# Optimization experiments

Hardware: AMD Instinct MI355X
Metric: run time of the kernel (lower is better)

The kernel has to match this reference:

```python
import jax, jax.numpy as jnp
import numpy as np

HEAD, DIM, R = 8, 256, 3
RA = (2 * R + 1) ** 2  # 49


def conv2d(x, w, b=None, pad=0, groups=1):
    y = jax.lax.conv_general_dilated(x, w, (1, 1), [(pad, pad), (pad, pad)],
                                     dimension_numbers=('NCHW', 'OIHW', 'NCHW'),
                                     feature_group_count=groups)
    return y if b is None else y + b[None, :, None, None]


def grid_sample(img, grid, mode, padding='zeros'):
    # img [B,C,H,W]; grid [B,Hg,Wg,2] with (x,y) in [-1,1]; align_corners=False.
    B, C, H, W = img.shape
    Hg, Wg = grid.shape[1], grid.shape[2]
    gx = ((grid[..., 0] + 1.0) * W - 1.0) / 2.0
    gy = ((grid[..., 1] + 1.0) * H - 1.0) / 2.0
    if padding == 'border':
        gx = jnp.clip(gx, 0.0, W - 1.0)
        gy = jnp.clip(gy, 0.0, H - 1.0)
    gx = gx.reshape(B, -1)
    gy = gy.reshape(B, -1)

    def gather(iy, ix):
        iyc = jnp.clip(iy, 0, H - 1)
        ixc = jnp.clip(ix, 0, W - 1)
        return jax.vmap(lambda im, a, b: im[:, a, b])(img, iyc, ixc)  # [B,C,N]

    def mask(iy, ix):
        if padding == 'border':
            return jnp.ones(iy.shape, img.dtype)
        return ((ix >= 0) & (ix < W) & (iy >= 0) & (iy < H)).astype(img.dtype)

    if mode == 'nearest':
        ix = jnp.round(gx).astype(jnp.int32)
        iy = jnp.round(gy).astype(jnp.int32)
        out = gather(iy, ix) * mask(iy, ix)[:, None, :]
    else:  # bilinear
        x0f = jnp.floor(gx); y0f = jnp.floor(gy)
        wx = gx - x0f; wy = gy - y0f
        x0 = x0f.astype(jnp.int32); y0 = y0f.astype(jnp.int32)
        out = jnp.zeros((B, C, gx.shape[1]), img.dtype)
        for dx, dy, w in ((0, 0, (1 - wx) * (1 - wy)), (1, 0, wx * (1 - wy)),
                          (0, 1, (1 - wx) * wy), (1, 1, wx * wy)):
            ix = x0 + dx; iy = y0 + dy
            out = out + gather(iy, ix) * (w * mask(iy, ix))[:, None, :]
    return out.reshape(B, C, Hg, Wg)


def mlp2(x, W1, b1, W2, b2):
    return jax.nn.relu(x @ W1.T + b1) @ W2.T + b2


def setup_inputs() -> dict:
    key = jax.random.key(0)
    ks = jax.random.split(key, 32)
    B, H, W, Q = 1, 64, 64, 4096
    f32 = jnp.float32
    rn = lambda k, shp, s=0.02: jax.random.normal(k, shp, f32) * s
    return {
        'inp': jax.random.normal(ks[0], (B, 3, H, W), f32),
        'coord': jax.random.uniform(ks[1], (B, Q, 2), f32, -1.0, 1.0),
        'cell': jnp.full((B, Q, 2), 2.0 / (2 * H), f32),
        'W_enc': rn(ks[2], (64, 3, 3, 3)), 'b_enc': jnp.zeros((64,), f32),
        'W_ch': rn(ks[3], (256, 64, 3, 3)), 'b_ch': jnp.zeros((256,), f32),
        'W_q': rn(ks[4], (256, 256, 3, 3)), 'b_q': jnp.zeros((256,), f32),
        'W_k': rn(ks[5], (256, 256, 3, 3)), 'b_k': jnp.zeros((256,), f32),
        'W_v': rn(ks[6], (256, 256, 3, 3)), 'b_v': jnp.zeros((256,), f32),
        'W_off1': rn(ks[7], (256, 32, 5, 5)), 'b_off1': jnp.zeros((256,), f32),
        'ln_g': jnp.ones((256,), f32), 'ln_b': jnp.zeros((256,), f32),
        'W_off2': rn(ks[8], (98, 256, 1, 1)),
        'Wc1': rn(ks[9], (256, 98)), 'bc1': jnp.zeros((256,), f32),
        'Wc2': rn(ks[10], (49, 256)), 'bc2': jnp.zeros((49,), f32),
        'Wi1': rn(ks[11], (256, 12546)), 'bi1': jnp.zeros((256,), f32),
        'Wi2': rn(ks[12], (3, 256)), 'bi2': jnp.zeros((3,), f32),
        'scale': 2,
    }


def reference(inp, coord, cell, W_enc, b_enc, W_ch, b_ch, W_q, b_q, W_k, b_k,
              W_v, b_v, W_off1, b_off1, ln_g, ln_b, W_off2, Wc1, bc1, Wc2, bc2,
              Wi1, bi1, Wi2, bi2, scale):
    B, _, H, W = inp.shape
    Q = coord.shape[1]
    # gen_feat: encoder stub (conv+relu) -> conv_ch -> q/k/v convs
    feat = conv2d(jax.nn.relu(conv2d(inp, W_enc, b_enc, pad=1)), W_ch, b_ch, pad=1)
    fq = conv2d(feat, W_q, b_q, pad=1)
    fk = conv2d(feat, W_k, b_k, pad=1)
    fv = conv2d(feat, W_v, b_v, pad=1)
    # offset branch: grouped 5x5 conv -> channelwise LN -> GELU -> 1x1 conv (no bias)
    o = conv2d(feat, W_off1, b_off1, pad=2, groups=8)
    oc = o.transpose(0, 2, 3, 1)
    mu = oc.mean(-1, keepdims=True)
    var = ((oc - mu) ** 2).mean(-1, keepdims=True)
    oc = (oc - mu) / jnp.sqrt(var + 1e-5) * ln_g + ln_b
    offsets = conv2d(jax.nn.gelu(oc.transpose(0, 3, 1, 2), approximate=False), W_off2, None, pad=0)  # [B,98,H,W]
    # LR coordinate grid (y,x) at pixel centers in [-1,1]
    ys = -1.0 + 1.0 / H + (2.0 / H) * jnp.arange(H, dtype=inp.dtype)
    xs = -1.0 + 1.0 / W + (2.0 / W) * jnp.arange(W, dtype=inp.dtype)
    coord_lr = jnp.broadcast_to(jnp.stack(jnp.meshgrid(ys, xs, indexing='ij'), 0)[None], (B, 2, H, W))
    sc = coord[:, :, None, :]          # [B,Q,1,2] (y,x)
    g = sc[..., ::-1]                  # (x,y) for grid_sample
    sck = grid_sample(coord_lr, g, 'nearest').transpose(0, 2, 3, 1)  # [B,Q,1,2]
    off = grid_sample(offsets, g, 'nearest').transpose(0, 2, 3, 1).reshape(B, Q, RA, 2)
    off = jnp.tanh(off) * jnp.array([1.0 / (H - 1.0), 1.0 / (W - 1.0)], inp.dtype) * 2.0
    d = jnp.linspace(-R, R, 2 * R + 1).astype(inp.dtype)
    delta = jnp.stack(jnp.meshgrid(d * (2.0 / H), d * (2.0 / W), indexing='ij'), -1).reshape(1, 1, RA, 2)
    sck = sck + delta + off            # [B,Q,49,2] sampling locs (y,x)
    q = grid_sample(fq, g, 'bilinear').transpose(0, 2, 3, 1).reshape(B, Q, HEAD, DIM // HEAD)
    k = grid_sample(fk, sck[..., ::-1], 'nearest').transpose(0, 2, 3, 1).reshape(B, Q, RA, HEAD, DIM // HEAD)
    v = grid_sample(fv, sck[..., ::-1], 'nearest').transpose(0, 2, 3, 1).reshape(B, Q, RA, HEAD, DIM // HEAD)
    attn_val = jnp.einsum('bqhd,bqkhd->bqkh', q, k) / np.sqrt(DIM // HEAD)  # [B,Q,49,8]
    rel = (sc - sck) * jnp.array([H, W], inp.dtype)  # [B,Q,49,2]
    wcoord = mlp2(rel.reshape(B * Q, RA * 2), Wc1, bc1, Wc2, bc2).reshape(B, Q, RA, 1)
    attn = jax.nn.softmax(wcoord + attn_val, axis=2)  # softmax over 49 samples
    feat_in = (v * attn[..., None]).reshape(B, Q, RA * DIM)
    rel_cell = cell * jnp.array([H, W], inp.dtype)
    feat_in = jnp.concatenate([feat_in, rel_cell], -1)  # [B,Q,12546]
    pred = mlp2(feat_in.reshape(B * Q, -1), Wi1, bi1, Wi2, bi2).reshape(B, Q, 3)
    skip = grid_sample(inp, g, 'bilinear', 'border')[:, :, :, 0].transpose(0, 2, 1)
    return pred + skip
```

## Files before the change

kernel.cpp:

```cpp
#include <hip/hip_runtime.h>
#include <hip/hip_bf16.h>


typedef unsigned short u16;
typedef unsigned int u32;
using frag_ab = __attribute__((ext_vector_type(8))) short;
using frag_cd = __attribute__((ext_vector_type(4))) float;

#define HW 4096
#define NQ 4096
#define KBIG 12576
#define SPLITK 16
#define KCHUNK 800
#define KQ 2304
#define QSPLIT 2
#define QCHUNK 1152

static __device__ __forceinline__ u16 f2b(float f) {
  union { __hip_bfloat16 h; u16 u; } c; c.h = __float2bfloat16(f); return c.u;
}
static __device__ __forceinline__ u32 pk2(float a, float b) {
  union { __hip_bfloat162 h; u32 u; } c;
  c.h = __float22bfloat162_rn(float2{a, b});
  return c.u;
}
static __device__ __forceinline__ void glds16(const u16* g, u16* l) {
  __builtin_amdgcn_global_load_lds(
      (const __attribute__((address_space(1))) u32*)(g),
      (__attribute__((address_space(3))) u32*)(l), 16, 0, 0);
}

#define BM 64
#define BN 64
#define BK 32
#define LDSS 40

__global__ __launch_bounds__(256)
void gemm_bt(const u16* __restrict__ A, const u16* __restrict__ Bt,
             void* __restrict__ Cv, const float* __restrict__ bias,
             int N, int K, int ldc, int flags,
             long sA, long sB, long sC, int sBias)
{
  __shared__ u16 As[BM * LDSS];
  __shared__ u16 Bs[BN * LDSS];
  const int z = blockIdx.z;
  A  += (long)z * sA;
  Bt += (long)z * sB;
  const float* bz = bias ? bias + (long)z * sBias : nullptr;

  const int tid  = threadIdx.x;
  const int m0   = blockIdx.x * BM;
  const int n0   = blockIdx.y * BN;
  const int wave = tid >> 6, lane = tid & 63;
  const int mw = (wave & 1) * 32, nw = (wave >> 1) * 32;
  const int lr = lane & 15, lk = lane >> 4;
  const int srow = tid >> 2, scol = (tid & 3) * 8;

  frag_cd acc[2][2] = {};
  const u16* aptr = A + (size_t)(m0 + srow) * K + scol;
  const bool bok  = (n0 + srow) < N;
  const u16* bptr = Bt + (size_t)(n0 + srow) * K + scol;

  uint4 av = *(const uint4*)(aptr);
  uint4 bv = bok ? *(const uint4*)(bptr) : uint4{0u, 0u, 0u, 0u};

  for (int k0 = 0; k0 < K; k0 += BK) {
    *(uint4*)&As[srow * LDSS + scol] = av;
    *(uint4*)&Bs[srow * LDSS + scol] = bv;
    __syncthreads();
    if (k0 + BK < K) {
      av = *(const uint4*)(aptr + k0 + BK);
      bv = bok ? *(const uint4*)(bptr + k0 + BK) : uint4{0u, 0u, 0u, 0u};
    }
    frag_ab af0 = *(const frag_ab*)&As[(mw      + lr) * LDSS + lk * 8];
    frag_ab af1 = *(const frag_ab*)&As[(mw + 16 + lr) * LDSS + lk * 8];
    frag_ab bf0 = *(const frag_ab*)&Bs[(nw      + lr) * LDSS + lk * 8];
    frag_ab bf1 = *(const frag_ab*)&Bs[(nw + 16 + lr) * LDSS + lk * 8];
    acc[0][0] = __builtin_amdgcn_mfma_f32_16x16x32_bf16(af0, bf0, acc[0][0], 0, 0, 0);
    acc[0][1] = __builtin_amdgcn_mfma_f32_16x16x32_bf16(af0, bf1, acc[0][1], 0, 0, 0);
    acc[1][0] = __builtin_amdgcn_mfma_f32_16x16x32_bf16(af1, bf0, acc[1][0], 0, 0, 0);
    acc[1][1] = __builtin_amdgcn_mfma_f32_16x16x32_bf16(af1, bf1, acc[1][1], 0, 0, 0);
    __syncthreads();
  }

  const bool relu = flags & 1;
  const bool obf  = flags & 2;
  #pragma unroll
  for (int i = 0; i < 2; i++)
    #pragma unroll
    for (int j = 0; j < 2; j++) {
      int col = n0 + nw + j * 16 + lr;
      if (col >= N) continue;
      float badd = bz ? bz[col] : 0.f;
      #pragma unroll
      for (int r = 0; r < 4; r++) {
        int row = m0 + mw + i * 16 + lk * 4 + r;
        float v = acc[i][j][r] + badd;
        if (relu) v = fmaxf(v, 0.f);
        size_t idx = (size_t)z * sC + (size_t)row * ldc + col;
        if (obf) ((u16*)Cv)[idx] = f2b(v);
        else     ((float*)Cv)[idx] = v;
      }
    }
}

template<int W3, int SH, int PAD>
__global__ __launch_bounds__(256)
void gemm_conv(const u16* __restrict__ feat, const u16* __restrict__ Bt,
               void* __restrict__ Cv, const float* __restrict__ bias,
               int N, int K, int ldc, int flags, int FC, int cbStride,
               long sB, long sC, int sBias)
{
  __shared__ u16 As[BM * LDSS];
  __shared__ u16 Bs[BN * LDSS];
  const int z = blockIdx.z;
  Bt += (long)z * sB;
  const float* bz = bias ? bias + (long)z * sBias : nullptr;
  const int cb = z * cbStride;

  const int tid  = threadIdx.x;
  const int m0   = blockIdx.x * BM;
  const int n0   = blockIdx.y * BN;
  const int wave = tid >> 6, lane = tid & 63;
  const int mw = (wave & 1) * 32, nw = (wave >> 1) * 32;
  const int lr = lane & 15, lk = lane >> 4;
  const int srow = tid >> 2, scol = (tid & 3) * 8;
  const int p = m0 + srow, y = p >> 6, x = p & 63;

  frag_cd acc[2][2] = {};
  const bool bok  = (n0 + srow) < N;
  const u16* bptr = Bt + (size_t)(n0 + srow) * K + scol;

  auto stageA = [&](int k0) -> uint4 {
    int k = k0 + scol;
    int s = k >> SH;
    int c = k & ((1 << SH) - 1);
    int dy = s / W3, dx = s - dy * W3;
    int yy = y + dy - PAD, xx = x + dx - PAD;
    if (((unsigned)yy < 64u) && ((unsigned)xx < 64u))
      return *(const uint4*)&feat[(size_t)(yy * 64 + xx) * FC + cb + c];
    return uint4{0u, 0u, 0u, 0u};
  };

  uint4 av = stageA(0);
  uint4 bv = bok ? *(const uint4*)(bptr) : uint4{0u, 0u, 0u, 0u};

  for (int k0 = 0; k0 < K; k0 += BK) {
    *(uint4*)&As[srow * LDSS + scol] = av;
    *(uint4*)&Bs[srow * LDSS + scol] = bv;
    __syncthreads();
    if (k0 + BK < K) {
      av = stageA(k0 + BK);
      bv = bok ? *(const uint4*)(bptr + k0 + BK) : uint4{0u, 0u, 0u, 0u};
    }
    frag_ab af0 = *(const frag_ab*)&As[(mw      + lr) * LDSS + lk * 8];
    frag_ab af1 = *(const frag_ab*)&As[(mw + 16 + lr) * LDSS + lk * 8];
    frag_ab bf0 = *(const frag_ab*)&Bs[(nw      + lr) * LDSS + lk * 8];
    frag_ab bf1 = *(const frag_ab*)&Bs[(nw + 16 + lr) * LDSS + lk * 8];
    acc[0][0] = __builtin_amdgcn_mfma_f32_16x16x32_bf16(af0, bf0, acc[0][0], 0, 0, 0);
    acc[0][1] = __builtin_amdgcn_mfma_f32_16x16x32_bf16(af0, bf1, acc[0][1], 0, 0, 0);
    acc[1][0] = __builtin_amdgcn_mfma_f32_16x16x32_bf16(af1, bf0, acc[1][0], 0, 0, 0);
    acc[1][1] = __builtin_amdgcn_mfma_f32_16x16x32_bf16(af1, bf1, acc[1][1], 0, 0, 0);
    __syncthreads();
  }

  const bool relu = flags & 1;
  const bool obf  = flags & 2;
  #pragma unroll
  for (int i = 0; i < 2; i++)
    #pragma unroll
    for (int j = 0; j < 2; j++) {
      int col = n0 + nw + j * 16 + lr;
      if (col >= N) continue;
      float badd = bz ? bz[col] : 0.f;
      #pragma unroll
      for (int r = 0; r < 4; r++) {
        int row = m0 + mw + i * 16 + lk * 4 + r;
        float v = acc[i][j][r] + badd;
        if (relu) v = fmaxf(v, 0.f);
        size_t idx = (size_t)z * sC + (size_t)row * ldc + col;
        if (obf) ((u16*)Cv)[idx] = f2b(v);
        else     ((float*)Cv)[idx] = v;
      }
    }
}

__global__ __launch_bounds__(256)
void gemm_qkv(const u16* __restrict__ feat, const u16* __restrict__ Bt,
              float* __restrict__ P)
{
  __shared__ u16 As[64 * LDSS];
  __shared__ u16 Bs[128 * 32];
  const int tid  = threadIdx.x;
  const int m0   = blockIdx.x * 64;
  const int n0   = blockIdx.y * 128;
  const int z    = blockIdx.z;
  const int kbeg = z * QCHUNK;
  const int kend = kbeg + QCHUNK;
  const int wave = tid >> 6, lane = tid & 63;
  const int nw = wave * 32;
  const int lr = lane & 15, lk = lane >> 4;
  const int arow = tid >> 2, acol = (tid & 3) * 8;
  const int p = m0 + arow, y = p >> 6, x = p & 63;

  frag_cd acc[4][2] = {};
  const u16* bbase = Bt + (size_t)(n0 + (tid >> 2)) * KQ + (tid & 3) * 8 + kbeg;
  u16* bdst = &Bs[(size_t)tid * 8];

  auto stageA = [&](int k0) -> uint4 {
    int k = k0 + acol;
    int s = k >> 8, c = k & 255;
    int dy = s / 3, dx = s - dy * 3;
    int yy = y + dy - 1, xx = x + dx - 1;
    if (((unsigned)yy < 64u) && ((unsigned)xx < 64u))
      return *(const uint4*)&feat[(size_t)(yy * 64 + xx) * 256 + c];
    return uint4{0u, 0u, 0u, 0u};
  };

  uint4 av = stageA(kbeg);

  for (int k0 = kbeg; k0 < kend; k0 += BK) {
    glds16(bbase + (k0 - kbeg), bdst);
    glds16(bbase + (k0 - kbeg) + (size_t)64 * KQ, bdst + 2048);
    *(uint4*)&As[arow * LDSS + acol] = av;
    __syncthreads();
    if (k0 + BK < kend) av = stageA(k0 + BK);
    frag_ab af[4];
    #pragma unroll
    for (int i = 0; i < 4; i++)
      af[i] = *(const frag_ab*)&As[(i * 16 + lr) * LDSS + lk * 8];
    #pragma unroll
    for (int j = 0; j < 2; j++) {
      frag_ab bf = *(const frag_ab*)&Bs[(nw + j * 16 + lr) * 32 + lk * 8];
      #pragma unroll
      for (int i = 0; i < 4; i++)
        acc[i][j] = __builtin_amdgcn_mfma_f32_16x16x32_bf16(af[i], bf, acc[i][j], 0, 0, 0);
    }
    __syncthreads();
  }

  #pragma unroll
  for (int i = 0; i < 4; i++)
    #pragma unroll
    for (int j = 0; j < 2; j++) {
      int col = n0 + nw + j * 16 + lr;
      #pragma unroll
      for (int r = 0; r < 4; r++) {
        int row = m0 + i * 16 + lk * 4 + r;
        P[(size_t)z * (NQ * 768) + (size_t)row * 768 + col] = acc[i][j][r];
      }
    }
}

__global__ __launch_bounds__(256)
void gemm_big(const u16* __restrict__ Bt, const float* __restrict__ fqkv,
              const float* __restrict__ attnval, const int* __restrict__ vidx,
              const float* __restrict__ cell, float* __restrict__ P)
{
  __shared__ u16 As[64 * LDSS];
  __shared__ u16 Bs[256 * 32];
  __shared__ int   s_vidx[5 * 64];
  __shared__ float s_attn[5 * 64 * 8];
  const int tid  = threadIdx.x;
  const int m0   = blockIdx.x * 64;
  const int z    = blockIdx.y;
  const int kbeg = z * KCHUNK;
  const int kend = min(KBIG, kbeg + KCHUNK);
  const int jbeg = kbeg >> 8;
  const int jcnt = ((kend - 1) >> 8) - jbeg + 1;
  const int wave = tid >> 6, lane = tid & 63;
  const int nw = wave * 64;
  const int lr = lane & 15, lk = lane >> 4;
  const int arow = tid >> 2, acol = (tid & 3) * 8;
  const int q = m0 + arow;

  for (int t = tid; t < 64 * jcnt; t += 256) {
    int r = t & 63, jj = t >> 6;
    int j = jbeg + jj;
    s_vidx[t] = (j < 49) ? vidx[(m0 + r) * 49 + j] : -1;
  }
  for (int t = tid; t < 64 * 8 * jcnt; t += 256) {
    int h = t & 7, rr = (t >> 3) & 63, jj = t >> 9;
    int j = jbeg + jj;
    s_attn[t] = (j < 49) ? attnval[((size_t)((m0 + rr) * 49 + j)) * 8 + h] : 0.f;
  }
  __syncthreads();

  auto stageA = [&](int k0) -> uint4 {
    const int k = k0 + acol;
    const int j = k >> 8, c = k & 255;
    union { u32 w[4]; uint4 v; } r; r.v = uint4{0u, 0u, 0u, 0u};
    if (j < 49) {
      const int jj = j - jbeg;
      int id = s_vidx[jj * 64 + arow];
      if (id >= 0) {
        float w = s_attn[(jj * 64 + arow) * 8 + (c >> 5)];
        const float* src = fqkv + (size_t)id * 768 + 512 + c;
        float4 f0 = *(const float4*)src;
        float4 f1 = *(const float4*)(src + 4);
        r.w[0] = pk2(f0.x * w, f0.y * w);
        r.w[1] = pk2(f0.z * w, f0.w * w);
        r.w[2] = pk2(f1.x * w, f1.y * w);
        r.w[3] = pk2(f1.z * w, f1.w * w);
      }
    } else if (c == 0) {
      r.w[0] = pk2(cell[q * 2] * 64.f, cell[q * 2 + 1] * 64.f);
    }
    return r.v;
  };

  frag_cd acc[4][4] = {};
  uint4 av = stageA(kbeg);
  const u16* bbase = Bt + (size_t)(tid >> 2) * KBIG + (tid & 3) * 8 + kbeg;
  u16* bdst = &Bs[(size_t)tid * 8];

  for (int k0 = kbeg; k0 < kend; k0 += BK) {
    #pragma unroll
    for (int i = 0; i < 4; i++)
      glds16(bbase + (k0 - kbeg) + (size_t)(i * 64) * KBIG, bdst + i * 2048);
    *(uint4*)&As[arow * LDSS + acol] = av;
    __syncthreads();
    if (k0 + BK < kend) av = stageA(k0 + BK);
    frag_ab af[4];
    #pragma unroll
    for (int i = 0; i < 4; i++)
      af[i] = *(const frag_ab*)&As[(i * 16 + lr) * LDSS + lk * 8];
    #pragma unroll
    for (int j = 0; j < 4; j++) {
      frag_ab bf = *(const frag_ab*)&Bs[(nw + j * 16 + lr) * 32 + lk * 8];
      #pragma unroll
      for (int i = 0; i < 4; i++)
        acc[i][j] = __builtin_amdgcn_mfma_f32_16x16x32_bf16(af[i], bf, acc[i][j], 0, 0, 0);
    }
    __syncthreads();
  }

  #pragma unroll
  for (int i = 0; i < 4; i++)
    #pragma unroll
    for (int j = 0; j < 4; j++) {
      int col = nw + j * 16 + lr;
      #pragma unroll
      for (int r = 0; r < 4; r++) {
        int row = m0 + i * 16 + lk * 4 + r;
        P[(size_t)z * (NQ * 256) + (size_t)row * 256 + col] = acc[i][j][r];
      }
    }
}

__global__ __launch_bounds__(256)
void reduce_sk4(const float* __restrict__ P, float* __restrict__ C,
                u16* __restrict__ Cb, const float* __restrict__ bias,
                int MN4, int N, int S, int relu)
{
  int i4 = blockIdx.x * 256 + threadIdx.x;
  if (i4 >= MN4) return;
  size_t i = (size_t)i4 * 4;
  float4 s = {0.f, 0.f, 0.f, 0.f};
  for (int zz = 0; zz < S; zz++) {
    float4 v = *(const float4*)&P[(size_t)zz * MN4 * 4 + i];
    s.x += v.x; s.y += v.y; s.z += v.z; s.w += v.w;
  }
  int c = (int)(i % N);
  s.x += bias[c]; s.y += bias[c + 1]; s.z += bias[c + 2]; s.w += bias[c + 3];
  if (relu) {
    s.x = fmaxf(s.x, 0.f); s.y = fmaxf(s.y, 0.f);
    s.z = fmaxf(s.z, 0.f); s.w = fmaxf(s.w, 0.f);
  }
  *(float4*)&C[i] = s;
  if (Cb) {
    uint2 pb = {pk2(s.x, s.y), pk2(s.z, s.w)};
    *(uint2*)&Cb[i] = pb;
  }
}

static __device__ __forceinline__
void packconv(const float* __restrict__ W, u16* __restrict__ Bt,
              int Cin, int K2, int idx)
{
  int o  = idx / (Cin * K2);
  int r  = idx - o * (Cin * K2);
  int ci = r / K2;
  int s  = r - ci * K2;
  Bt[(size_t)o * (Cin * K2) + s * Cin + ci] = f2b(W[idx]);
}
static __device__ __forceinline__
void packcast(const float* __restrict__ W, u16* __restrict__ Bt,
              int Kin, int Kout, int idx)
{
  int n = idx / Kout, k = idx - n * Kout;
  Bt[idx] = f2b(k < Kin ? W[(size_t)n * Kin + k] : 0.f);
}

#define SZ_CH   147456
#define SZ_QKV  589824
#define SZ_OFF1 204800
#define SZ_OFF2 25088
#define SZ_C1   32768
#define SZ_C2   12544
#define SZ_PACK (SZ_CH + 3*SZ_QKV + SZ_OFF1 + SZ_OFF2 + SZ_C1 + SZ_C2 + 768)

__global__ void pack_misc(const float* W_ch, const float* W_q, const float* W_k,
                          const float* W_v, const float* W_off1, const float* W_off2,
                          const float* Wc1, const float* Wc2,
                          const float* b_q, const float* b_k, const float* b_v,
                          u16* Btch, u16* Btqkv, u16* Btoff1, u16* Btoff2,
                          u16* Btc1, u16* Btc2, float* bqkv)
{
  int i = blockIdx.x * 256 + threadIdx.x;
  if (i < SZ_CH) { packconv(W_ch, Btch, 64, 9, i); return; }
  i -= SZ_CH;
  if (i < SZ_QKV) { packconv(W_q, Btqkv, 256, 9, i); return; }
  i -= SZ_QKV;
  if (i < SZ_QKV) { packconv(W_k, Btqkv + (size_t)256 * 2304, 256, 9, i); return; }
  i -= SZ_QKV;
  if (i < SZ_QKV) { packconv(W_v, Btqkv + (size_t)512 * 2304, 256, 9, i); return; }
  i -= SZ_QKV;
  if (i < SZ_OFF1) { packconv(W_off1, Btoff1, 32, 25, i); return; }
  i -= SZ_OFF1;
  if (i < SZ_OFF2) { packcast(W_off2, Btoff2, 256, 256, i); return; }
  i -= SZ_OFF2;
  if (i < SZ_C1) { packcast(Wc1, Btc1, 98, 128, i); return; }
  i -= SZ_C1;
  if (i < SZ_C2) { packcast(Wc2, Btc2, 256, 256, i); return; }
  i -= SZ_C2;
  if (i < 768) {
    bqkv[i] = (i < 256) ? b_q[i] : (i < 512) ? b_k[i - 256] : b_v[i - 512];
  }
}

__global__ void pack_cast(const float* __restrict__ W, u16* __restrict__ Bt,
                          int N, int Kin, int Kout)
{
  int idx = blockIdx.x * 256 + threadIdx.x;
  if (idx >= N * Kout) return;
  int n = idx / Kout, k = idx - n * Kout;
  Bt[idx] = f2b(k < Kin ? W[(size_t)n * Kin + k] : 0.f);
}

__global__ __launch_bounds__(64)
void conv_enc(const float* __restrict__ inp, const float* __restrict__ W,
              const float* __restrict__ b, u16* __restrict__ feat1)
{
  const int p = blockIdx.x, c = threadIdx.x;
  const int y = p >> 6, x = p & 63;
  float s = b[c];
  #pragma unroll
  for (int ci = 0; ci < 3; ci++)
    #pragma unroll
    for (int dy = 0; dy < 3; dy++) {
      int yy = y + dy - 1;
      if ((unsigned)yy >= 64u) continue;
      #pragma unroll
      for (int dx = 0; dx < 3; dx++) {
        int xx = x + dx - 1;
        if ((unsigned)xx >= 64u) continue;
        s += inp[ci * HW + yy * 64 + xx] * W[((c * 3 + ci) * 3 + dy) * 3 + dx];
      }
    }
  feat1[(size_t)p * 64 + c] = f2b(fmaxf(s, 0.f));
}

__global__ __launch_bounds__(256)
void ln_gelu(const float* __restrict__ x, const float* __restrict__ g,
             const float* __restrict__ b, u16* __restrict__ y)
{
  const int p = blockIdx.x, c = threadIdx.x;
  __shared__ float r1[4], r2[4];
  float v = x[(size_t)p * 256 + c];
  float s1 = v, s2 = v * v;
  #pragma unroll
  for (int off = 32; off; off >>= 1) {
    s1 += __shfl_xor(s1, off);
    s2 += __shfl_xor(s2, off);
  }
  if ((c & 63) == 0) { r1[c >> 6] = s1; r2[c >> 6] = s2; }
  __syncthreads();
  float t1 = r1[0] + r1[1] + r1[2] + r1[3];
  float t2 = r2[0] + r2[1] + r2[2] + r2[3];
  float mu  = t1 * (1.f / 256.f);
  float var = t2 * (1.f / 256.f) - mu * mu;
  float xn = (v - mu) * rsqrtf(var + 1e-5f) * g[c] + b[c];
  float ge = 0.5f * xn * (1.f + erff(xn * 0.70710678118654752f));
  y[(size_t)p * 256 + c] = f2b(ge);
}

__global__ __launch_bounds__(256)
void sampler(const float* __restrict__ coord, const float* __restrict__ fqkv,
             const u16* __restrict__ fqkvb, const float* __restrict__ offs,
             const float* __restrict__ inp, float* __restrict__ attnval,
             u16* __restrict__ relbuf, int* __restrict__ vidx,
             float* __restrict__ skipb)
{
  const int q = blockIdx.x;
  const int tid = threadIdx.x;
  __shared__ float s_off[98];
  __shared__ int s_idx[49];
  __shared__ float s_q[256];

  const float c0 = coord[q * 2], c1 = coord[q * 2 + 1];
  const float gxp = ((c1 + 1.f) * 64.f - 1.f) * 0.5f;
  const float gyp = ((c0 + 1.f) * 64.f - 1.f) * 0.5f;
  const int ixn = (int)rintf(gxp), iyn = (int)rintf(gyp);
  const bool inn = ((unsigned)ixn < 64u) && ((unsigned)iyn < 64u);

  if (tid < 98) {
    float v = inn ? offs[(size_t)(iyn * 64 + ixn) * 98 + tid] : 0.f;
    s_off[tid] = tanhf(v) * (2.f / 63.f);
  }
  __syncthreads();

  const float scky = inn ? (-1.f + (float)(2 * iyn + 1) * (1.f / 64.f)) : 0.f;
  const float sckx = inn ? (-1.f + (float)(2 * ixn + 1) * (1.f / 64.f)) : 0.f;

  if (tid < 49) {
    const int a = tid / 7, bb = tid - a * 7;
    float sy = scky + (float)(a - 3) * (2.f / 64.f) + s_off[2 * tid];
    float sx = sckx + (float)(bb - 3) * (2.f / 64.f) + s_off[2 * tid + 1];
    relbuf[(size_t)q * 128 + 2 * tid]     = f2b((c0 - sy) * 64.f);
    relbuf[(size_t)q * 128 + 2 * tid + 1] = f2b((c1 - sx) * 64.f);
    float gx2 = ((sx + 1.f) * 64.f - 1.f) * 0.5f;
    float gy2 = ((sy + 1.f) * 64.f - 1.f) * 0.5f;
    int ix2 = (int)rintf(gx2), iy2 = (int)rintf(gy2);
    int id = (((unsigned)ix2 < 64u) && ((unsigned)iy2 < 64u)) ? (iy2 * 64 + ix2) : -1;
    s_idx[tid] = id;
    vidx[q * 49 + tid] = id;
  } else if (tid >= 98 && tid < 128) {
    relbuf[(size_t)q * 128 + tid] = 0;
  }

  {
    const float x0f = floorf(gxp), y0f = floorf(gyp);
    const float wx = gxp - x0f, wy = gyp - y0f;
    const int x0 = (int)x0f, y0 = (int)y0f;
    float qc = 0.f;
    #pragma unroll
    for (int t = 0; t < 4; t++) {
      int xi = x0 + (t & 1), yi = y0 + (t >> 1);
      if (((unsigned)xi < 64u) && ((unsigned)yi < 64u)) {
        float w = ((t & 1) ? wx : 1.f - wx) * ((t >> 1) ? wy : 1.f - wy);
        qc += w * fqkv[(size_t)(yi * 64 + xi) * 768 + tid];
      }
    }
    s_q[tid] = qc * 0.17677669529663687f;
  }

  if (tid < 3) {
    float gx = fminf(fmaxf(gxp, 0.f), 63.f);
    float gy = fminf(fmaxf(gyp, 0.f), 63.f);
    float xf = floorf(gx), yf = floorf(gy);
    float wxs = gx - xf, wys = gy - yf;
    int xa = (int)xf, ya = (int)yf;
    int xb = min(xa + 1, 63), yb = min(ya + 1, 63);
    const float* ch = inp + tid * HW;
    float v = (1.f - wxs) * (1.f - wys) * ch[ya * 64 + xa]
            + wxs * (1.f - wys) * ch[ya * 64 + xb]
            + (1.f - wxs) * wys * ch[yb * 64 + xa]
            + wxs * wys * ch[yb * 64 + xb];
    skipb[q * 3 + tid] = v;
  }
  __syncthreads();

  const int wave = tid >> 6, lane = tid & 63;
  const int half = lane >> 5, sub = lane & 31;
  const int ch0 = sub * 8;
  const int h = sub >> 2;
  float qv[8];
  #pragma unroll
  for (int i = 0; i < 8; i++) qv[i] = s_q[ch0 + i];

  for (int it = 0; it < 7; it++) {
    int j = it * 8 + wave * 2 + half;
    if (j >= 49) break;
    int id = s_idx[j];
    float p = 0.f;
    if (id >= 0) {
      uint4 kv = *(const uint4*)&fqkvb[(size_t)id * 768 + 256 + ch0];
      u32 w0 = kv.x, w1 = kv.y, w2 = kv.z, w3 = kv.w;
      p = fmaf(qv[0], __uint_as_float(w0 << 16), p);
      p = fmaf(qv[1], __uint_as_float(w0 & 0xffff0000u), p);
      p = fmaf(qv[2], __uint_as_float(w1 << 16), p);
      p = fmaf(qv[3], __uint_as_float(w1 & 0xffff0000u), p);
      p = fmaf(qv[4], __uint_as_float(w2 << 16), p);
      p = fmaf(qv[5], __uint_as_float(w2 & 0xffff0000u), p);
      p = fmaf(qv[6], __uint_as_float(w3 << 16), p);
      p = fmaf(qv[7], __uint_as_float(w3 & 0xffff0000u), p);
    }
    p += __shfl_down(p, 2, 4);
    p += __shfl_down(p, 1, 4);
    if ((sub & 3) == 0) attnval[((size_t)q * 49 + j) * 8 + h] = p;
  }
}

__global__ __launch_bounds__(512)
void softmax_k(const float* __restrict__ wc, float* __restrict__ attnval)
{
  const int q = blockIdx.x;
  const int tid = threadIdx.x;
  const int hh = tid >> 6, l = tid & 63;
  float v = (l < 49) ? wc[(size_t)q * 49 + l] + attnval[((size_t)q * 49 + l) * 8 + hh]
                     : -1e30f;
  float m = v;
  #pragma unroll
  for (int off = 32; off; off >>= 1) m = fmaxf(m, __shfl_xor(m, off));
  float e = (l < 49) ? expf(v - m) : 0.f;
  float s = e;
  #pragma unroll
  for (int off = 32; off; off >>= 1) s += __shfl_xor(s, off);
  if (l < 49) attnval[((size_t)q * 49 + l) * 8 + hh] = e / s;
}

__global__ __launch_bounds__(256)
void final_out(const float* __restrict__ hid2, const float* __restrict__ Wi2,
               const float* __restrict__ bi2, const float* __restrict__ skipb,
               float* __restrict__ out)
{
  const int q = blockIdx.x, c = threadIdx.x;
  __shared__ float part[3][4];
  float hv = hid2[(size_t)q * 256 + c];
  float p0 = hv * Wi2[c], p1 = hv * Wi2[256 + c], p2 = hv * Wi2[512 + c];
  #pragma unroll
  for (int off = 32; off; off >>= 1) {
    p0 += __shfl_xor(p0, off);
    p1 += __shfl_xor(p1, off);
    p2 += __shfl_xor(p2, off);
  }
  if ((c & 63) == 0) {
    int w = c >> 6;
    part[0][w] = p0; part[1][w] = p1; part[2][w] = p2;
  }
  __syncthreads();
  if (c < 3)
    out[q * 3 + c] = bi2[c] + skipb[q * 3 + c]
                   + part[c][0] + part[c][1] + part[c][2] + part[c][3];
}

extern "C" void kernel_launch(void* const* d_in, const int* in_sizes, int n_in,
                              void* d_out, int out_size, void* d_ws, size_t ws_size,
                              hipStream_t stream)
{
  const float* inp    = (const float*)d_in[0];
  const float* coord  = (const float*)d_in[1];
  const float* cell   = (const float*)d_in[2];
  const float* W_enc  = (const float*)d_in[3];
  const float* b_enc  = (const float*)d_in[4];
  const float* W_ch   = (const float*)d_in[5];
  const float* b_ch   = (const float*)d_in[6];
  const float* W_q    = (const float*)d_in[7];
  const float* b_q    = (const float*)d_in[8];
  const float* W_k    = (const float*)d_in[9];
  const float* b_k    = (const float*)d_in[10];
  const float* W_v    = (const float*)d_in[11];
  const float* b_v    = (const float*)d_in[12];
  const float* W_off1 = (const float*)d_in[13];
  const float* b_off1 = (const float*)d_in[14];
  const float* ln_g   = (const float*)d_in[15];
  const float* ln_b   = (const float*)d_in[16];
  const float* W_off2 = (const float*)d_in[17];
  const float* Wc1    = (const float*)d_in[18];
  const float* bc1    = (const float*)d_in[19];
  const float* Wc2    = (const float*)d_in[20];
  const float* bc2    = (const float*)d_in[21];
  const float* Wi1    = (const float*)d_in[22];
  const float* bi1    = (const float*)d_in[23];
  const float* Wi2    = (const float*)d_in[24];
  const float* bi2    = (const float*)d_in[25];

  char* base = (char*)d_ws;
  size_t off = 0;
  auto alloc = [&](size_t bytes) -> char* {
    char* r = base + off;
    off = (off + bytes + 255) & ~(size_t)255;
    return r;
  };

  float* obuf   = (float*)alloc((size_t)HW * 256 * 4);
  u16*   ocg    = (u16*)  alloc((size_t)HW * 256 * 2);
  float* offsb  = (float*)alloc((size_t)HW * 98 * 4);
  u16*   feat1  = (u16*)  alloc((size_t)HW * 64 * 2);
  u16*   feat   = (u16*)  alloc((size_t)HW * 256 * 2);
  u16*   hid1   = (u16*)  alloc((size_t)NQ * 256 * 2);
  float* wcb    = (float*)alloc((size_t)NQ * 49 * 4);
  u16*   relbuf = (u16*)  alloc((size_t)NQ * 128 * 2);
  u16*   Btqkv  = (u16*)  alloc((size_t)768 * 2304 * 2);
  u16*   Btch   = (u16*)  alloc((size_t)256 * 576 * 2);
  u16*   Btoff1 = (u16*)  alloc((size_t)256 * 800 * 2);
  u16*   Btoff2 = (u16*)  alloc((size_t)98 * 256 * 2);
  u16*   Btc1   = (u16*)  alloc((size_t)256 * 128 * 2);
  u16*   Btc2   = (u16*)  alloc((size_t)49 * 256 * 2);
  float* Pbuf = (float*)base;
  float* Pq = (float*)(base + ((size_t)36 << 20));
  {
    size_t need = (size_t)SPLITK * NQ * 256 * 4;
    if (off < need) off = (need + 255) & ~(size_t)255;
  }
  float* fqkv    = (float*)alloc((size_t)HW * 768 * 4);
  u16*   fqkvb   = (u16*)  alloc((size_t)HW * 768 * 2);
  float* attnval = (float*)alloc((size_t)NQ * 49 * 8 * 4);
  int*   vidxb   = (int*)  alloc((size_t)NQ * 49 * 4);
  float* skipb   = (float*)alloc((size_t)NQ * 3 * 4);
  float* hid2    = (float*)alloc((size_t)NQ * 256 * 4);
  u16*   Wi1p    = (u16*)  alloc((size_t)256 * KBIG * 2);
  float* bqkv    = (float*)alloc(768 * 4);
  (void)ws_size; (void)in_sizes; (void)n_in; (void)out_size;

  pack_misc<<<(SZ_PACK + 255) / 256, 256, 0, stream>>>(
      W_ch, W_q, W_k, W_v, W_off1, W_off2, Wc1, Wc2, b_q, b_k, b_v,
      Btch, Btqkv, Btoff1, Btoff2, Btc1, Btc2, bqkv);
  pack_cast<<<(256 * KBIG + 255) / 256, 256, 0, stream>>>(Wi1, Wi1p, 256, 12546, KBIG);

  conv_enc<<<HW, 64, 0, stream>>>(inp, W_enc, b_enc, feat1);
  gemm_conv<3, 6, 1><<<dim3(64, 4, 1), 256, 0, stream>>>(
      feat1, Btch, feat, b_ch, 256, 576, 256, 2, 64, 0, 0, 0, 0);
  gemm_qkv<<<dim3(64, 6, QSPLIT), 256, 0, stream>>>(feat, Btqkv, Pq);
  reduce_sk4<<<(NQ * 192 + 255) / 256, 256, 0, stream>>>(
      Pq, fqkv, fqkvb, bqkv, NQ * 192, 768, QSPLIT, 0);
  gemm_conv<5, 5, 2><<<dim3(64, 1, 8), 256, 0, stream>>>(
      feat, Btoff1, obuf, b_off1, 32, 800, 256, 0, 256, 32,
      (long)32 * 800, 32, 32);
  ln_gelu<<<HW, 256, 0, stream>>>(obuf, ln_g, ln_b, ocg);
  gemm_bt<<<dim3(64, 2, 1), 256, 0, stream>>>(ocg, Btoff2, offsb, nullptr,
      98, 256, 98, 0, 0, 0, 0, 0);

  sampler<<<NQ, 256, 0, stream>>>(coord, fqkv, fqkvb, offsb, inp,
                                  attnval, relbuf, vidxb, skipb);
  gemm_bt<<<dim3(64, 4, 1), 256, 0, stream>>>(relbuf, Btc1, hid1, bc1,
      256, 128, 256, 3, 0, 0, 0, 0);
  gemm_bt<<<dim3(64, 1, 1), 256, 0, stream>>>(hid1, Btc2, wcb, bc2,
      49, 256, 49, 0, 0, 0, 0, 0);
  softmax_k<<<NQ, 512, 0, stream>>>(wcb, attnval);

  gemm_big<<<dim3(64, SPLITK), 256, 0, stream>>>(
      Wi1p, fqkv, attnval, vidxb, cell, Pbuf);
  reduce_sk4<<<(NQ * 64 + 255) / 256, 256, 0, stream>>>(
      Pbuf, hid2, nullptr, bi1, NQ * 64, 256, SPLITK, 1);
  final_out<<<NQ, 256, 0, stream>>>(hid2, Wi2, bi2, skipb, (float*)d_out);
}
```

Baseline: 312.2 us.

## Store split-K partials in bf16, drop fp32 qkv copy, fuse final reduction

After: 318.9 us. +2.2%, slower.

```diff
diff --git a/kernel.cpp b/kernel.cpp
--- a/kernel.cpp
+++ b/kernel.cpp
@@ -18,6 +18,9 @@
 
 static __device__ __forceinline__ u16 f2b(float f) {
   union { __hip_bfloat16 h; u16 u; } c; c.h = __float2bfloat16(f); return c.u;
+}
+static __device__ __forceinline__ float b2f(u16 v) {
+  return __uint_as_float((u32)v << 16);
 }
 static __device__ __forceinline__ u32 pk2(float a, float b) {
   union { __hip_bfloat162 h; u32 u; } c;
@@ -187,7 +190,7 @@
 
 __global__ __launch_bounds__(256)
 void gemm_qkv(const u16* __restrict__ feat, const u16* __restrict__ Bt,
-              float* __restrict__ P)
+              u16* __restrict__ P)
 {
   __shared__ u16 As[64 * LDSS];
   __shared__ u16 Bs[128 * 32];
@@ -247,15 +250,39 @@
       #pragma unroll
       for (int r = 0; r < 4; r++) {
         int row = m0 + i * 16 + lk * 4 + r;
-        P[(size_t)z * (NQ * 768) + (size_t)row * 768 + col] = acc[i][j][r];
+        P[(size_t)z * (NQ * 768) + (size_t)row * 768 + col] = f2b(acc[i][j][r]);
       }
     }
 }
 
 __global__ __launch_bounds__(256)
-void gemm_big(const u16* __restrict__ Bt, const float* __restrict__ fqkv,
+void reduce_qkv(const u16* __restrict__ P, const float* __restrict__ bias,
+                u16* __restrict__ outb)
+{
+  int i8 = blockIdx.x * 256 + threadIdx.x;
+  if (i8 >= NQ * 96) return;
+  size_t i = (size_t)i8 * 8;
+  int c = (int)(i % 768);
+  uint4 a = *(const uint4*)&P[i];
+  uint4 b = *(const uint4*)&P[(size_t)NQ * 768 + i];
+  u32 aw[4] = {a.x, a.y, a.z, a.w};
+  u32 bw[4] = {b.x, b.y, b.z, b.w};
+  u32 ow[4];
+  #pragma unroll
+  for (int t = 0; t < 4; t++) {
+    float lo = __uint_as_float(aw[t] << 16) + __uint_as_float(bw[t] << 16)
+             + bias[c + 2 * t];
+    float hi = __uint_as_float(aw[t] & 0xffff0000u)
+             + __uint_as_float(bw[t] & 0xffff0000u) + bias[c + 2 * t + 1];
+    ow[t] = pk2(lo, hi);
+  }
+  *(uint4*)&outb[i] = uint4{ow[0], ow[1], ow[2], ow[3]};
+}
+
+__global__ __launch_bounds__(256)
+void gemm_big(const u16* __restrict__ Bt, const u16* __restrict__ fqkvb,
               const float* __restrict__ attnval, const int* __restrict__ vidx,
-              const float* __restrict__ cell, float* __restrict__ P)
+              const float* __restrict__ cell, u16* __restrict__ P)
 {
   __shared__ u16 As[64 * LDSS];
   __shared__ u16 Bs[256 * 32];
@@ -295,13 +322,15 @@
       int id = s_vidx[jj * 64 + arow];
       if (id >= 0) {
         float w = s_attn[(jj * 64 + arow) * 8 + (c >> 5)];
-        const float* src = fqkv + (size_t)id * 768 + 512 + c;
-        float4 f0 = *(const float4*)src;
-        float4 f1 = *(const float4*)(src + 4);
-        r.w[0] = pk2(f0.x * w, f0.y * w);
-        r.w[1] = pk2(f0.z * w, f0.w * w);
-        r.w[2] = pk2(f1.x * w, f1.y * w);
-        r.w[3] = pk2(f1.z * w, f1.w * w);
+        uint4 kv = *(const uint4*)&fqkvb[(size_t)id * 768 + 512 + c];
+        r.w[0] = pk2(__uint_as_float(kv.x << 16) * w,
+                     __uint_as_float(kv.x & 0xffff0000u) * w);
+        r.w[1] = pk2(__uint_as_float(kv.y << 16) * w,
+                     __uint_as_float(kv.y & 0xffff0000u) * w);
+        r.w[2] = pk2(__uint_as_float(kv.z << 16) * w,
+                     __uint_as_float(kv.z & 0xffff0000u) * w);
+        r.w[3] = pk2(__uint_as_float(kv.w << 16) * w,
+                     __uint_as_float(kv.w & 0xffff0000u) * w);
       }
     } else if (c == 0) {
       r.w[0] = pk2(cell[q * 2] * 64.f, cell[q * 2 + 1] * 64.f);
@@ -343,35 +372,40 @@
       #pragma unroll
       for (int r = 0; r < 4; r++) {
         int row = m0 + i * 16 + lk * 4 + r;
-        P[(size_t)z * (NQ * 256) + (size_t)row * 256 + col] = acc[i][j][r];
+        P[(size_t)z * (NQ * 256) + (size_t)row * 256 + col] = f2b(acc[i][j][r]);
       }
     }
 }
 
 __global__ __launch_bounds__(256)
-void reduce_sk4(const float* __restrict__ P, float* __restrict__ C,
-                u16* __restrict__ Cb, const float* __restrict__ bias,
-                int MN4, int N, int S, int relu)
-{
-  int i4 = blockIdx.x * 256 + threadIdx.x;
-  if (i4 >= MN4) return;
-  size_t i = (size_t)i4 * 4;
-  float4 s = {0.f, 0.f, 0.f, 0.f};
-  for (int zz = 0; zz < S; zz++) {
-    float4 v = *(const float4*)&P[(size_t)zz * MN4 * 4 + i];
-    s.x += v.x; s.y += v.y; s.z += v.z; s.w += v.w;
-  }
-  int c = (int)(i % N);
-  s.x += bias[c]; s.y += bias[c + 1]; s.z += bias[c + 2]; s.w += bias[c + 3];
-  if (relu) {
-    s.x = fmaxf(s.x, 0.f); s.y = fmaxf(s.y, 0.f);
-    s.z = fmaxf(s.z, 0.f); s.w = fmaxf(s.w, 0.f);
-  }
-  *(float4*)&C[i] = s;
-  if (Cb) {
-    uint2 pb = {pk2(s.x, s.y), pk2(s.z, s.w)};
-    *(uint2*)&Cb[i] = pb;
-  }
+void reduce_final(const u16* __restrict__ Pb, const float* __restrict__ bi1,
+                  const float* __restrict__ Wi2, const float* __restrict__ bi2,
+                  const float* __restrict__ skipb, float* __restrict__ out)
+{
+  const int q = blockIdx.x, c = threadIdx.x;
+  float s = 0.f;
+  #pragma unroll
+  for (int z = 0; z < SPLITK; z++)
+    s += b2f(Pb[(size_t)z * (NQ * 256) + (size_t)q * 256 + c]);
+  s += bi1[c];
+  s = fmaxf(s, 0.f);
+
+  __shared__ float part[3][4];
+  float p0 = s * Wi2[c], p1 = s * Wi2[256 + c], p2 = s * Wi2[512 + c];
+  #pragma unroll
+  for (int off = 32; off; off >>= 1) {
+    p0 += __shfl_xor(p0, off);
+    p1 += __shfl_xor(p1, off);
+    p2 += __shfl_xor(p2, off);
+  }
+  if ((c & 63) == 0) {
+    int w = c >> 6;
+    part[0][w] = p0; part[1][w] = p1; part[2][w] = p2;
+  }
+  __syncthreads();
+  if (c < 3)
+    out[q * 3 + c] = bi2[c] + skipb[q * 3 + c]
+                   + part[c][0] + part[c][1] + part[c][2] + part[c][3];
 }
 
 static __device__ __forceinline__
@@ -486,11 +520,10 @@
 }
 
 __global__ __launch_bounds__(256)
-void sampler(const float* __restrict__ coord, const float* __restrict__ fqkv,
-             const u16* __restrict__ fqkvb, const float* __restrict__ offs,
-             const float* __restrict__ inp, float* __restrict__ attnval,
-             u16* __restrict__ relbuf, int* __restrict__ vidx,
-             float* __restrict__ skipb)
+void sampler(const float* __restrict__ coord, const u16* __restrict__ fqkvb,
+             const float* __restrict__ offs, const float* __restrict__ inp,
+             float* __restrict__ attnval, u16* __restrict__ relbuf,
+             int* __restrict__ vidx, float* __restrict__ skipb)
 {
   const int q = blockIdx.x;
   const int tid = threadIdx.x;
@@ -539,7 +572,7 @@
       int xi = x0 + (t & 1), yi = y0 + (t >> 1);
       if (((unsigned)xi < 64u) && ((unsigned)yi < 64u)) {
         float w = ((t & 1) ? wx : 1.f - wx) * ((t >> 1) ? wy : 1.f - wy);
-        qc += w * fqkv[(size_t)(yi * 64 + xi) * 768 + tid];
+        qc += w * b2f(fqkvb[(size_t)(yi * 64 + xi) * 768 + tid]);
       }
     }
     s_q[tid] = qc * 0.17677669529663687f;
@@ -608,31 +641,6 @@
   #pragma unroll
   for (int off = 32; off; off >>= 1) s += __shfl_xor(s, off);
   if (l < 49) attnval[((size_t)q * 49 + l) * 8 + hh] = e / s;
-}
-
-__global__ __launch_bounds__(256)
-void final_out(const float* __restrict__ hid2, const float* __restrict__ Wi2,
-               const float* __restrict__ bi2, const float* __restrict__ skipb,
-               float* __restrict__ out)
-{
-  const int q = blockIdx.x, c = threadIdx.x;
-  __shared__ float part[3][4];
-  float hv = hid2[(size_t)q * 256 + c];
-  float p0 = hv * Wi2[c], p1 = hv * Wi2[256 + c], p2 = hv * Wi2[512 + c];
-  #pragma unroll
-  for (int off = 32; off; off >>= 1) {
-    p0 += __shfl_xor(p0, off);
-    p1 += __shfl_xor(p1, off);
-    p2 += __shfl_xor(p2, off);
-  }
-  if ((c & 63) == 0) {
-    int w = c >> 6;
-    part[0][w] = p0; part[1][w] = p1; part[2][w] = p2;
-  }
-  __syncthreads();
-  if (c < 3)
-    out[q * 3 + c] = bi2[c] + skipb[q * 3 + c]
-                   + part[c][0] + part[c][1] + part[c][2] + part[c][3];
 }
 
 extern "C" void kernel_launch(void* const* d_in, const int* in_sizes, int n_in,
@@ -688,18 +696,16 @@
   u16*   Btoff2 = (u16*)  alloc((size_t)98 * 256 * 2);
   u16*   Btc1   = (u16*)  alloc((size_t)256 * 128 * 2);
   u16*   Btc2   = (u16*)  alloc((size_t)49 * 256 * 2);
-  float* Pbuf = (float*)base;
-  float* Pq = (float*)(base + ((size_t)36 << 20));
+  u16* Pb = (u16*)base;
+  u16* Pqb = (u16*)(base + ((size_t)36 << 20));
   {
-    size_t need = (size_t)SPLITK * NQ * 256 * 4;
+    size_t need = ((size_t)36 << 20) + (size_t)QSPLIT * NQ * 768 * 2;
     if (off < need) off = (need + 255) & ~(size_t)255;
   }
-  float* fqkv    = (float*)alloc((size_t)HW * 768 * 4);
   u16*   fqkvb   = (u16*)  alloc((size_t)HW * 768 * 2);
   float* attnval = (float*)alloc((size_t)NQ * 49 * 8 * 4);
   int*   vidxb   = (int*)  alloc((size_t)NQ * 49 * 4);
   float* skipb   = (float*)alloc((size_t)NQ * 3 * 4);
-  float* hid2    = (float*)alloc((size_t)NQ * 256 * 4);
   u16*   Wi1p    = (u16*)  alloc((size_t)256 * KBIG * 2);
   float* bqkv    = (float*)alloc(768 * 4);
   (void)ws_size; (void)in_sizes; (void)n_in; (void)out_size;
@@ -712,9 +718,8 @@
   conv_enc<<<HW, 64, 0, stream>>>(inp, W_enc, b_enc, feat1);
   gemm_conv<3, 6, 1><<<dim3(64, 4, 1), 256, 0, stream>>>(
       feat1, Btch, feat, b_ch, 256, 576, 256, 2, 64, 0, 0, 0, 0);
-  gemm_qkv<<<dim3(64, 6, QSPLIT), 256, 0, stream>>>(feat, Btqkv, Pq);
-  reduce_sk4<<<(NQ * 192 + 255) / 256, 256, 0, stream>>>(
-      Pq, fqkv, fqkvb, bqkv, NQ * 192, 768, QSPLIT, 0);
+  gemm_qkv<<<dim3(64, 6, QSPLIT), 256, 0, stream>>>(feat, Btqkv, Pqb);
+  reduce_qkv<<<(NQ * 96 + 255) / 256, 256, 0, stream>>>(Pqb, bqkv, fqkvb);
   gemm_conv<5, 5, 2><<<dim3(64, 1, 8), 256, 0, stream>>>(
       feat, Btoff1, obuf, b_off1, 32, 800, 256, 0, 256, 32,
       (long)32 * 800, 32, 32);
@@ -722,7 +727,7 @@
   gemm_bt<<<dim3(64, 2, 1), 256, 0, stream>>>(ocg, Btoff2, offsb, nullptr,
       98, 256, 98, 0, 0, 0, 0, 0);
 
-  sampler<<<NQ, 256, 0, stream>>>(coord, fqkv, fqkvb, offsb, inp,
+  sampler<<<NQ, 256, 0, stream>>>(coord, fqkvb, offsb, inp,
                                   attnval, relbuf, vidxb, skipb);
   gemm_bt<<<dim3(64, 4, 1), 256, 0, stream>>>(relbuf, Btc1, hid1, bc1,
       256, 128, 256, 3, 0, 0, 0, 0);
@@ -731,8 +736,6 @@
   softmax_k<<<NQ, 512, 0, stream>>>(wcb, attnval);
 
   gemm_big<<<dim3(64, SPLITK), 256, 0, stream>>>(
-      Wi1p, fqkv, attnval, vidxb, cell, Pbuf);
-  reduce_sk4<<<(NQ * 64 + 255) / 256, 256, 0, stream>>>(
-      Pbuf, hid2, nullptr, bi1, NQ * 64, 256, SPLITK, 1);
-  final_out<<<NQ, 256, 0, stream>>>(hid2, Wi2, bi2, skipb, (float*)d_out);
-}
+      Wi1p, fqkvb, attnval, vidxb, cell, Pb);
+  reduce_final<<<NQ, 256, 0, stream>>>(Pb, bi1, Wi2, bi2, skipb, (float*)d_out);
+}
```
